# Optimization experiments

Measured on AMD Instinct MI355X. Metric: run time of the kernel, lower is better.

## Reference

```python
import jax, jax.numpy as jnp
import numpy as np

B, T, C = 2, 2048, 2048
NH, NKV, HD = 16, 8, 256
SOFTCAP = 50.0
ROPE_BASE = 10000.0


def setup_inputs() -> dict:
    key = jax.random.key(0)
    ks = jax.random.split(key, 5)
    s = 0.02
    return {
        "X": jax.random.normal(ks[0], (B, T, C), dtype=jnp.float32),
        "Wq": jax.random.normal(ks[1], (C, NH * HD), dtype=jnp.float32) * s,
        "Wk": jax.random.normal(ks[2], (C, NKV * HD), dtype=jnp.float32) * s,
        "Wv": jax.random.normal(ks[3], (C, NKV * HD), dtype=jnp.float32) * s,
        "Wo": jax.random.normal(ks[4], (NH * HD, C), dtype=jnp.float32) * s,
    }


def _rotate_half(x):
    x1, x2 = x[..., : x.shape[-1] // 2], x[..., x.shape[-1] // 2 :]
    return jnp.concatenate((-x2, x1), axis=-1)


def _rope_cos_sin(t, head_dim, dtype):
    inv_freq = 1.0 / ROPE_BASE ** (
        jnp.arange(0, head_dim, 2, dtype=jnp.int32).astype(jnp.float32) / head_dim
    )  # [HD/2]
    pos = jnp.arange(t, dtype=jnp.float32)  # [T]
    freqs = pos[:, None] * inv_freq[None, :]  # [T, HD/2]
    emb = jnp.concatenate((freqs, freqs), axis=-1)  # [T, HD]
    # shape [1, 1, T, HD] to broadcast over (B, H, T, HD)
    return (
        jnp.cos(emb).astype(dtype)[None, None],
        jnp.sin(emb).astype(dtype)[None, None],
    )


def reference(X, Wq, Wk, Wv, Wo):
    b, t, c = X.shape
    n_rep = NH // NKV

    q = (X @ Wq).reshape(b, t, NH, HD).transpose(0, 2, 1, 3)   # [B,NH,T,HD]
    k = (X @ Wk).reshape(b, t, NKV, HD).transpose(0, 2, 1, 3)  # [B,NKV,T,HD]
    v = (X @ Wv).reshape(b, t, NKV, HD).transpose(0, 2, 1, 3)

    cos, sin = _rope_cos_sin(t, HD, X.dtype)
    q = q * cos + _rotate_half(q) * sin
    k = k * cos + _rotate_half(k) * sin

    # repeat_kv (GQA): [B,NKV,T,HD] -> [B,NH,T,HD]
    k = jnp.repeat(k, n_rep, axis=1)
    v = jnp.repeat(v, n_rep, axis=1)

    scale = 256.0 ** (-0.5)  # hardcoded in source
    att = jnp.einsum("bhqd,bhkd->bhqk", q, k) * scale
    # tanh logit softcapping
    att = SOFTCAP * jnp.tanh(att / SOFTCAP)
    # causal mask
    causal = jnp.tril(jnp.ones((t, t), dtype=bool))
    att = jnp.where(causal[None, None], att, -jnp.inf)
    att = jax.nn.softmax(att, axis=-1)

    y = jnp.einsum("bhqk,bhkd->bhqd", att, v)  # [B,NH,T,HD]
    y = y.transpose(0, 2, 1, 3).reshape(b, t, NH * HD)
    return y @ Wo
```

## Files before the change

### kernel.cpp

```cpp
#include <hip/hip_runtime.h>
#include <hip/hip_bf16.h>

#define NHD 16
#define NKVH 8
#define HDIM 256
#define TSEQ 2048
#define BATCH 2

typedef unsigned int   u32;
typedef unsigned short u16;

typedef __attribute__((ext_vector_type(8))) short bf16x8;
typedef __attribute__((ext_vector_type(4))) float floatx4;

__device__ inline u32 cvt2bf(float lo, float hi) {
  u32 r;
  asm("v_cvt_pk_bf16_f32 %0, %1, %2" : "=v"(r) : "v"(lo), "v"(hi));
  return r;
}
__device__ inline u16 f2bf(float f) {
  union { float f; u32 i; } v; v.f = f;
  u32 r = v.i + 0x7fffu + ((v.i >> 16) & 1u);
  return (u16)(r >> 16);
}
__device__ inline float bf2f(u16 u) {
  union { u32 i; float f; } v; v.i = ((u32)u) << 16; return v.f;
}
__device__ inline float fexp2(float x) {
  float r; asm("v_exp_f32 %0, %1" : "=v"(r) : "v"(x)); return r;
}
__device__ inline float frcp(float x) {
  float r; asm("v_rcp_f32 %0, %1" : "=v"(r) : "v"(x)); return r;
}

typedef const __attribute__((address_space(1))) u32* gptr_t;
typedef __attribute__((address_space(3))) u32* lptr_t;
__device__ inline void gl_lds16(const void* g, void* l) {
  __builtin_amdgcn_global_load_lds((gptr_t)g, (lptr_t)l, 16, 0, 0);
}

__global__ __launch_bounds__(256) void tconv_k(
    const float* __restrict__ in, u16* __restrict__ out, int R, int Cc)
{
  __shared__ float tile[64][65];
  const int r0 = blockIdx.y * 64, c0 = blockIdx.x * 64;
  const int tr = threadIdx.x >> 4;
  const int tc = (threadIdx.x & 15) * 4;
#pragma unroll
  for (int j = 0; j < 4; ++j) {
    float4 v = *(const float4*)(in + (size_t)(r0 + tr + j * 16) * Cc + c0 + tc);
    tile[tr + j * 16][tc + 0] = v.x;
    tile[tr + j * 16][tc + 1] = v.y;
    tile[tr + j * 16][tc + 2] = v.z;
    tile[tr + j * 16][tc + 3] = v.w;
  }
  __syncthreads();
#pragma unroll
  for (int j = 0; j < 4; ++j) {
    int c = tr + j * 16;
    u16 o[4];
#pragma unroll
    for (int i = 0; i < 4; ++i) o[i] = f2bf(tile[tc + i][c]);
    *(uint2*)(out + (size_t)(c0 + c) * R + r0 + tc) = *(const uint2*)o;
  }
}

__global__ __launch_bounds__(256) void xconv_k(
    const float* __restrict__ in, u16* __restrict__ out)
{
  size_t i = (size_t)blockIdx.x * 256 + threadIdx.x;
  float4 a = *(const float4*)(in + i * 8);
  float4 b = *(const float4*)(in + i * 8 + 4);
  uint4 o;
  o.x = cvt2bf(a.x, a.y); o.y = cvt2bf(a.z, a.w);
  o.z = cvt2bf(b.x, b.y); o.w = cvt2bf(b.z, b.w);
  *(uint4*)(out + i * 8) = o;
}

template<int EPI, int BM>
__global__ __launch_bounds__(512, 2) void gemm256_k(
    const u16* __restrict__ Ab, const u16* __restrict__ BTp,
    void* __restrict__ Op, int M, int N, int K)
{
  constexpr int NI = BM / 32;
  constexpr int AI = BM / 64;
  __shared__ u16 LA[2][BM * 64];
  __shared__ u16 LB[2][256 * 64];
  const int t = threadIdx.x;
  const int lane = t & 63, wave = t >> 6;
  const int lg = lane >> 4, l15 = lane & 15;
  const int wm = wave >> 2, wn = wave & 3;
  const int mtiles = M / BM;
  const int mt = (int)blockIdx.x % mtiles, nt = (int)blockIdx.x / mtiles;
  const int m0 = mt * BM, n0 = nt << 8;

  const int arow = wave * (BM / 8) + (lane >> 3);
  const int ska  = ((lane & 7) ^ (arow & 7)) << 3;
  const int brow = wave * 32 + (lane >> 3);
  const int skb  = ((lane & 7) ^ (brow & 7)) << 3;
  const u16* Ag = Ab  + (size_t)(m0 + arow) * K + ska;
  const u16* Bg = BTp + (size_t)(n0 + brow) * K + skb;

  auto STAGE = [&](int k0, int sel) {
#pragma unroll
    for (int q = 0; q < AI; ++q)
      gl_lds16(Ag + k0 + (size_t)q * 8 * K, &LA[sel][(wave * (BM / 8) + q * 8) * 64]);
#pragma unroll
    for (int q = 0; q < 4; ++q)
      gl_lds16(Bg + k0 + (size_t)q * 8 * K, &LB[sel][(wave * 32 + q * 8) * 64]);
  };

  floatx4 acc[NI][4];
#pragma unroll
  for (int i = 0; i < NI; ++i)
#pragma unroll
    for (int j = 0; j < 4; ++j) acc[i][j] = (floatx4){0.f, 0.f, 0.f, 0.f};

  STAGE(0, 0);
  const int KT = K >> 6;
  for (int kt = 0; kt < KT; ++kt) {
    const int sel = kt & 1;
    if (kt + 1 < KT) {
      STAGE((kt + 1) << 6, sel ^ 1);
      if constexpr (BM == 256) asm volatile("s_waitcnt vmcnt(8)" ::: "memory");
      else                     asm volatile("s_waitcnt vmcnt(6)" ::: "memory");
    } else {
      asm volatile("s_waitcnt vmcnt(0)" ::: "memory");
    }
    __builtin_amdgcn_s_barrier();
    __builtin_amdgcn_sched_barrier(0);
    __builtin_amdgcn_s_setprio(1);
#pragma unroll
    for (int ks = 0; ks < 2; ++ks) {
      const int c = (ks << 2) + lg;
      bf16x8 bfv[4];
#pragma unroll
      for (int j = 0; j < 4; ++j) {
        int row = wn * 64 + (j << 4) + l15;
        bfv[j] = *(const bf16x8*)(&LB[sel][row * 64 + ((c ^ (row & 7)) << 3)]);
      }
#pragma unroll
      for (int i = 0; i < NI; ++i) {
        int row = wm * (BM / 2) + (i << 4) + l15;
        bf16x8 af = *(const bf16x8*)(&LA[sel][row * 64 + ((c ^ (row & 7)) << 3)]);
#pragma unroll
        for (int j = 0; j < 4; ++j)
          acc[i][j] = __builtin_amdgcn_mfma_f32_16x16x32_bf16(af, bfv[j], acc[i][j], 0, 0, 0);
      }
    }
    __builtin_amdgcn_s_setprio(0);
    __builtin_amdgcn_s_barrier();
  }

#pragma unroll
  for (int i = 0; i < NI; ++i) {
#pragma unroll
    for (int j = 0; j < 4; ++j) {
#pragma unroll
      for (int r = 0; r < 4; ++r) {
        int m = m0 + wm * (BM / 2) + (i << 4) + (lg << 2) + r;
        int n = n0 + wn * 64 + (j << 4) + l15;
        float v = acc[i][j][r];
        int bb = m >> 11, tt = m & 2047;
        if (EPI == 0) {
          ((float*)Op)[(size_t)m * N + n] = v;
        } else if (EPI == 1) {
          int h = n >> 8, d = n & 255;
          ((u16*)Op)[(((size_t)bb * NHD + h) * TSEQ + tt) * HDIM + d] = f2bf(v);
        } else {
          if (n < 2048) {
            int h = n >> 8, d = n & 255;
            ((u16*)Op)[(((size_t)bb * NKVH + h) * TSEQ + tt) * HDIM + d] = f2bf(v);
          } else {
            int n2 = n - 2048;
            int h = n2 >> 8, d = n2 & 255;
            ((u16*)Op)[8388608u + (((size_t)bb * NKVH + h) * HDIM + d) * TSEQ + tt] = f2bf(v);
          }
        }
      }
    }
  }
}

__global__ __launch_bounds__(256) void rope_k(u16* buf) {
  size_t idx = (size_t)blockIdx.x * 256 + threadIdx.x;
  int d = (int)(idx & 127);
  size_t rest = idx >> 7;
  int tt = (int)(rest & (TSEQ - 1));
  float invf = exp2f(-(float)d * 0.103810253f);
  float th = (float)tt * invf;
  float sn, cs;
  sincosf(th, &sn, &cs);
  size_t base = rest * HDIM;
  float x1 = bf2f(buf[base + d]);
  float x2 = bf2f(buf[base + d + 128]);
  buf[base + d]       = f2bf(x1 * cs - x2 * sn);
  buf[base + d + 128] = f2bf(x2 * cs + x1 * sn);
}

__global__ __launch_bounds__(256, 2) void attn_k(
    const u16* __restrict__ Q, const u16* __restrict__ Kb,
    const u16* __restrict__ Vt, u16* __restrict__ Y)
{
  __shared__ u16 Ks2[2][32 * 256];
  __shared__ u16 Vs2[2][256 * 32];
  __shared__ u16 Ps[4 * 16 * 32];
  __shared__ float Ls[4][16];
  const int t = threadIdx.x, lane = t & 63, w = t >> 6;
  const int lg = lane >> 4, l15 = lane & 15;
  const int qt = 31 - (int)blockIdx.y;
  const int h = (int)blockIdx.x >> 1, b = (int)blockIdx.x & 1;
  const int hkv = h >> 1;

  const u16* Kg = Kb + ((size_t)(b * NKVH + hkv)) * TSEQ * HDIM;
  const u16* Vg = Vt + ((size_t)(b * NKVH + hkv)) * HDIM * TSEQ;

  int koff[4], voff[4];
#pragma unroll
  for (int q = 0; q < 4; ++q) {
    int krow = w * 8 + q * 2 + (lane >> 5);
    int kcc  = lane & 31;
    koff[q] = krow * 256 + ((kcc ^ (krow & 7)) << 3);
    int vd  = w * 64 + q * 16 + (lane >> 2);
    voff[q] = vd * TSEQ + (((lane & 3) ^ ((vd >> 2) & 3)) << 3);
  }

  auto STAGE = [&](int st, int sel) {
    const u16* kbase = Kg + (size_t)st * (32 * 256);
    const u16* vbase = Vg + st * 32;
#pragma unroll
    for (int q = 0; q < 4; ++q)
      gl_lds16(kbase + koff[q], &Ks2[sel][(w * 8 + q * 2) * 256]);
#pragma unroll
    for (int q = 0; q < 4; ++q)
      gl_lds16(vbase + voff[q], &Vs2[sel][(w * 64 + q * 16) * 32]);
  };

  const u16* Qg = Q + (((size_t)(b * NHD + h)) * TSEQ + qt * 64 + w * 16 + l15) * HDIM;
  bf16x8 qf[8];
#pragma unroll
  for (int ks = 0; ks < 8; ++ks) qf[ks] = *(const bf16x8*)(Qg + ks * 32 + lg * 8);

  floatx4 accY[16];
#pragma unroll
  for (int i = 0; i < 16; ++i) accY[i] = (floatx4){0.f, 0.f, 0.f, 0.f};
  float rsum = 0.f;

  const int qglob = qt * 64 + w * 16 + l15;
  const int qmaxw = qt * 64 + w * 16 + 15;
  const int nst = 2 * qt + 2;
  const int fps = (l15 ^ (l15 >> 2)) & 3;

  STAGE(0, 0);
  for (int st = 0; st < nst; ++st) {
    const int sel = st & 1;
    if (st + 1 < nst) {
      STAGE(st + 1, sel ^ 1);
      asm volatile("s_waitcnt vmcnt(8)" ::: "memory");
    } else {
      asm volatile("s_waitcnt vmcnt(0)" ::: "memory");
    }
    __builtin_amdgcn_s_barrier();
    __builtin_amdgcn_sched_barrier(0);

    if (st * 32 <= qmaxw) {
      __builtin_amdgcn_s_setprio(1);
#pragma unroll
      for (int stile = 0; stile < 2; ++stile) {
        floatx4 sa = (floatx4){0.f, 0.f, 0.f, 0.f};
#pragma unroll
        for (int ks = 0; ks < 8; ++ks) {
          int row = (stile << 4) + l15;
          int c = (ks << 2) + lg;
          bf16x8 kf = *(const bf16x8*)((const char*)Ks2[sel] +
                        row * 512 + ((c ^ (row & 7)) << 4));
          sa = __builtin_amdgcn_mfma_f32_16x16x32_bf16(kf, qf[ks], sa, 0, 0, 0);
        }
        int sbase = st * 32 + (stile << 4) + (lg << 2);
        float p[4];
#pragma unroll
        for (int r = 0; r < 4; ++r) {
          float u = fexp2(sa[r] * 0.0036067376f);
          float pv = fexp2(-144.26950408f * frcp(u + 1.0f));
          pv = (sbase + r <= qglob) ? pv : 0.0f;
          p[r] = pv;
          rsum += pv;
        }
        uint2 pw;
        pw.x = cvt2bf(p[0], p[1]);
        pw.y = cvt2bf(p[2], p[3]);
        int o = (stile << 5) + (lg << 3);
        int gran = (o >> 4) ^ fps;
        *(uint2*)((char*)Ps + (w << 10) + l15 * 64 + (gran << 4) + (o & 15)) = pw;
      }
      {
        bf16x8 pf = *(const bf16x8*)((const char*)Ps + (w << 10) + l15 * 64 +
                      ((lg ^ fps) << 4));
#pragma unroll
        for (int dt = 0; dt < 16; ++dt) {
          int row = (dt << 4) + l15;
          bf16x8 vf = *(const bf16x8*)((const char*)Vs2[sel] +
                        row * 64 + ((lg ^ ((row >> 2) & 3)) << 4));
          accY[dt] = __builtin_amdgcn_mfma_f32_16x16x32_bf16(pf, vf, accY[dt], 0, 0, 0);
        }
      }
      __builtin_amdgcn_s_setprio(0);
    }
    __builtin_amdgcn_s_barrier();
  }

  rsum += __shfl_xor(rsum, 16);
  rsum += __shfl_xor(rsum, 32);
  if (lane < 16) Ls[w][l15] = rsum;
  __syncthreads();
  float inv[4];
#pragma unroll
  for (int r = 0; r < 4; ++r) inv[r] = 1.0f / Ls[w][(lg << 2) + r];

  u16* Yg = Y + ((size_t)(b * TSEQ + qt * 64 + w * 16)) * (NHD * HDIM) + h * HDIM;
#pragma unroll
  for (int dt = 0; dt < 16; ++dt)
#pragma unroll
    for (int r = 0; r < 4; ++r)
      Yg[(size_t)((lg << 2) + r) * (NHD * HDIM) + (dt << 4) + l15] =
          f2bf(accY[dt][r] * inv[r]);
}

extern "C" void kernel_launch(void* const* d_in, const int* in_sizes, int n_in,
                              void* d_out, int out_size, void* d_ws, size_t ws_size,
                              hipStream_t stream) {
  const float* X  = (const float*)d_in[0];
  const float* Wq = (const float*)d_in[1];
  const float* Wk = (const float*)d_in[2];
  const float* Wv = (const float*)d_in[3];
  const float* Wo = (const float*)d_in[4];
  float* out = (float*)d_out;

  u16* ws   = (u16*)d_ws;
  u16* XB   = ws;
  u16* WT   = ws + 8388608;
  u16* Qb   = ws + 16777216;
  u16* KVb  = ws + 33554432;
  u16* Yb   = ws;
  u16* WoT  = ws + 16777216;

  dim3 blk(256);
  xconv_k<<<dim3(4096), blk, 0, stream>>>(X, XB);
  tconv_k<<<dim3(64, 32), blk, 0, stream>>>(Wq, WT, 2048, 4096);
  gemm256_k<1, 256><<<dim3(16 * 16), dim3(512), 0, stream>>>(XB, WT, Qb, 4096, 4096, 2048);
  tconv_k<<<dim3(32, 32), blk, 0, stream>>>(Wk, WT, 2048, 2048);
  tconv_k<<<dim3(32, 32), blk, 0, stream>>>(Wv, WT + (size_t)2048 * 2048, 2048, 2048);
  gemm256_k<3, 256><<<dim3(16 * 16), dim3(512), 0, stream>>>(XB, WT, KVb, 4096, 4096, 2048);
  rope_k<<<dim3((BATCH * NHD  * TSEQ * 128) / 256), blk, 0, stream>>>(Qb);
  rope_k<<<dim3((BATCH * NKVH * TSEQ * 128) / 256), blk, 0, stream>>>(KVb);
  attn_k<<<dim3(32, 32), blk, 0, stream>>>(Qb, KVb, KVb + 8388608, Yb);
  tconv_k<<<dim3(32, 64), blk, 0, stream>>>(Wo, WoT, 4096, 2048);
  gemm256_k<0, 128><<<dim3(32 * 8), dim3(512), 0, stream>>>(Yb, WoT, out, 4096, 2048, 4096);
}
```

Baseline: 424.9 us.

## Share K/V tiles across both GQA query heads and split GEMM B-tile staging

The attention kernel now processes both query heads that share a KV head in one block. Each staged K/V tile is reused twice and the grid is halved, which cuts global K/V traffic and staging work. This doubles the Q fragment and Y accumulator registers per thread, so occupancy may drop or registers may spill. Separately, the GEMM prefetch now issues the next A tile before compute and the next B tile between the two k-substeps. The vmcnt waits are adjusted to match, so load issue interleaves with MFMA work.

Result: slower. 680.7 us (+60.2%).

```diff
diff --git a/kernel.cpp b/kernel.cpp
--- a/kernel.cpp
+++ b/kernel.cpp
@@ -101,10 +101,12 @@
   const u16* Ag = Ab  + (size_t)(m0 + arow) * K + ska;
   const u16* Bg = BTp + (size_t)(n0 + brow) * K + skb;
 
-  auto STAGE = [&](int k0, int sel) {
+  auto STAGE_A = [&](int k0, int sel) {
 #pragma unroll
     for (int q = 0; q < AI; ++q)
       gl_lds16(Ag + k0 + (size_t)q * 8 * K, &LA[sel][(wave * (BM / 8) + q * 8) * 64]);
+  };
+  auto STAGE_B = [&](int k0, int sel) {
 #pragma unroll
     for (int q = 0; q < 4; ++q)
       gl_lds16(Bg + k0 + (size_t)q * 8 * K, &LB[sel][(wave * 32 + q * 8) * 64]);
@@ -116,23 +118,46 @@
 #pragma unroll
     for (int j = 0; j < 4; ++j) acc[i][j] = (floatx4){0.f, 0.f, 0.f, 0.f};
 
-  STAGE(0, 0);
+  STAGE_A(0, 0);
+  STAGE_B(0, 0);
   const int KT = K >> 6;
   for (int kt = 0; kt < KT; ++kt) {
     const int sel = kt & 1;
     if (kt + 1 < KT) {
-      STAGE((kt + 1) << 6, sel ^ 1);
-      if constexpr (BM == 256) asm volatile("s_waitcnt vmcnt(8)" ::: "memory");
-      else                     asm volatile("s_waitcnt vmcnt(6)" ::: "memory");
+      STAGE_A((kt + 1) << 6, sel ^ 1);
+      if constexpr (BM == 256) asm volatile("s_waitcnt vmcnt(4)" ::: "memory");
+      else                     asm volatile("s_waitcnt vmcnt(2)" ::: "memory");
     } else {
       asm volatile("s_waitcnt vmcnt(0)" ::: "memory");
     }
     __builtin_amdgcn_s_barrier();
     __builtin_amdgcn_sched_barrier(0);
+
     __builtin_amdgcn_s_setprio(1);
-#pragma unroll
-    for (int ks = 0; ks < 2; ++ks) {
-      const int c = (ks << 2) + lg;
+    {
+      const int c = lg;
+      bf16x8 bfv[4];
+#pragma unroll
+      for (int j = 0; j < 4; ++j) {
+        int row = wn * 64 + (j << 4) + l15;
+        bfv[j] = *(const bf16x8*)(&LB[sel][row * 64 + ((c ^ (row & 7)) << 3)]);
+      }
+#pragma unroll
+      for (int i = 0; i < NI; ++i) {
+        int row = wm * (BM / 2) + (i << 4) + l15;
+        bf16x8 af = *(const bf16x8*)(&LA[sel][row * 64 + ((c ^ (row & 7)) << 3)]);
+#pragma unroll
+        for (int j = 0; j < 4; ++j)
+          acc[i][j] = __builtin_amdgcn_mfma_f32_16x16x32_bf16(af, bfv[j], acc[i][j], 0, 0, 0);
+      }
+    }
+    __builtin_amdgcn_s_setprio(0);
+
+    if (kt + 1 < KT) STAGE_B((kt + 1) << 6, sel ^ 1);
+
+    __builtin_amdgcn_s_setprio(1);
+    {
+      const int c = 4 + lg;
       bf16x8 bfv[4];
 #pragma unroll
       for (int j = 0; j < 4; ++j) {
@@ -205,12 +230,11 @@
   __shared__ u16 Ks2[2][32 * 256];
   __shared__ u16 Vs2[2][256 * 32];
   __shared__ u16 Ps[4 * 16 * 32];
-  __shared__ float Ls[4][16];
+  __shared__ float Ls[4][2][16];
   const int t = threadIdx.x, lane = t & 63, w = t >> 6;
   const int lg = lane >> 4, l15 = lane & 15;
   const int qt = 31 - (int)blockIdx.y;
-  const int h = (int)blockIdx.x >> 1, b = (int)blockIdx.x & 1;
-  const int hkv = h >> 1;
+  const int hkv = (int)blockIdx.x >> 1, b = (int)blockIdx.x & 1;
 
   const u16* Kg = Kb + ((size_t)(b * NKVH + hkv)) * TSEQ * HDIM;
   const u16* Vg = Vt + ((size_t)(b * NKVH + hkv)) * HDIM * TSEQ;
@@ -236,15 +260,22 @@
       gl_lds16(vbase + voff[q], &Vs2[sel][(w * 64 + q * 16) * 32]);
   };
 
-  const u16* Qg = Q + (((size_t)(b * NHD + h)) * TSEQ + qt * 64 + w * 16 + l15) * HDIM;
-  bf16x8 qf[8];
-#pragma unroll
-  for (int ks = 0; ks < 8; ++ks) qf[ks] = *(const bf16x8*)(Qg + ks * 32 + lg * 8);
-
-  floatx4 accY[16];
-#pragma unroll
-  for (int i = 0; i < 16; ++i) accY[i] = (floatx4){0.f, 0.f, 0.f, 0.f};
-  float rsum = 0.f;
+  bf16x8 qf[2][8];
+#pragma unroll
+  for (int u = 0; u < 2; ++u) {
+    const u16* Qg = Q + (((size_t)(b * NHD + 2 * hkv + u)) * TSEQ +
+                         qt * 64 + w * 16 + l15) * HDIM;
+#pragma unroll
+    for (int ks = 0; ks < 8; ++ks)
+      qf[u][ks] = *(const bf16x8*)(Qg + ks * 32 + lg * 8);
+  }
+
+  floatx4 accY[2][16];
+#pragma unroll
+  for (int u = 0; u < 2; ++u)
+#pragma unroll
+    for (int i = 0; i < 16; ++i) accY[u][i] = (floatx4){0.f, 0.f, 0.f, 0.f};
+  float rsum[2] = {0.f, 0.f};
 
   const int qglob = qt * 64 + w * 16 + l15;
   const int qmaxw = qt * 64 + w * 16 + 15;
@@ -266,64 +297,74 @@
     if (st * 32 <= qmaxw) {
       __builtin_amdgcn_s_setprio(1);
 #pragma unroll
-      for (int stile = 0; stile < 2; ++stile) {
-        floatx4 sa = (floatx4){0.f, 0.f, 0.f, 0.f};
-#pragma unroll
-        for (int ks = 0; ks < 8; ++ks) {
-          int row = (stile << 4) + l15;
-          int c = (ks << 2) + lg;
-          bf16x8 kf = *(const bf16x8*)((const char*)Ks2[sel] +
-                        row * 512 + ((c ^ (row & 7)) << 4));
-          sa = __builtin_amdgcn_mfma_f32_16x16x32_bf16(kf, qf[ks], sa, 0, 0, 0);
+      for (int u = 0; u < 2; ++u) {
+#pragma unroll
+        for (int stile = 0; stile < 2; ++stile) {
+          floatx4 sa = (floatx4){0.f, 0.f, 0.f, 0.f};
+#pragma unroll
+          for (int ks = 0; ks < 8; ++ks) {
+            int row = (stile << 4) + l15;
+            int c = (ks << 2) + lg;
+            bf16x8 kf = *(const bf16x8*)((const char*)Ks2[sel] +
+                          row * 512 + ((c ^ (row & 7)) << 4));
+            sa = __builtin_amdgcn_mfma_f32_16x16x32_bf16(kf, qf[u][ks], sa, 0, 0, 0);
+          }
+          int sbase = st * 32 + (stile << 4) + (lg << 2);
+          float p[4];
+#pragma unroll
+          for (int r = 0; r < 4; ++r) {
+            float uu = fexp2(sa[r] * 0.0036067376f);
+            float pv = fexp2(-144.26950408f * frcp(uu + 1.0f));
+            pv = (sbase + r <= qglob) ? pv : 0.0f;
+            p[r] = pv;
+            rsum[u] += pv;
+          }
+          uint2 pw;
+          pw.x = cvt2bf(p[0], p[1]);
+          pw.y = cvt2bf(p[2], p[3]);
+          int o = (stile << 5) + (lg << 3);
+          int gran = (o >> 4) ^ fps;
+          *(uint2*)((char*)Ps + (w << 10) + l15 * 64 + (gran << 4) + (o & 15)) = pw;
         }
-        int sbase = st * 32 + (stile << 4) + (lg << 2);
-        float p[4];
-#pragma unroll
-        for (int r = 0; r < 4; ++r) {
-          float u = fexp2(sa[r] * 0.0036067376f);
-          float pv = fexp2(-144.26950408f * frcp(u + 1.0f));
-          pv = (sbase + r <= qglob) ? pv : 0.0f;
-          p[r] = pv;
-          rsum += pv;
+        {
+          bf16x8 pf = *(const bf16x8*)((const char*)Ps + (w << 10) + l15 * 64 +
+                        ((lg ^ fps) << 4));
+#pragma unroll
+          for (int dt = 0; dt < 16; ++dt) {
+            int row = (dt << 4) + l15;
+            bf16x8 vf = *(const bf16x8*)((const char*)Vs2[sel] +
+                          row * 64 + ((lg ^ ((row >> 2) & 3)) << 4));
+            accY[u][dt] = __builtin_amdgcn_mfma_f32_16x16x32_bf16(pf, vf, accY[u][dt], 0, 0, 0);
+          }
         }
-        uint2 pw;
-        pw.x = cvt2bf(p[0], p[1]);
-        pw.y = cvt2bf(p[2], p[3]);
-        int o = (stile << 5) + (lg << 3);
-        int gran = (o >> 4) ^ fps;
-        *(uint2*)((char*)Ps + (w << 10) + l15 * 64 + (gran << 4) + (o & 15)) = pw;
-      }
-      {
-        bf16x8 pf = *(const bf16x8*)((const char*)Ps + (w << 10) + l15 * 64 +
-                      ((lg ^ fps) << 4));
-#pragma unroll
-        for (int dt = 0; dt < 16; ++dt) {
-          int row = (dt << 4) + l15;
-          bf16x8 vf = *(const bf16x8*)((const char*)Vs2[sel] +
-                        row * 64 + ((lg ^ ((row >> 2) & 3)) << 4));
-          accY[dt] = __builtin_amdgcn_mfma_f32_16x16x32_bf16(pf, vf, accY[dt], 0, 0, 0);
-        }
       }
       __builtin_amdgcn_s_setprio(0);
     }
     __builtin_amdgcn_s_barrier();
   }
 
-  rsum += __shfl_xor(rsum, 16);
-  rsum += __shfl_xor(rsum, 32);
-  if (lane < 16) Ls[w][l15] = rsum;
+#pragma unroll
+  for (int u = 0; u < 2; ++u) {
+    float rs = rsum[u];
+    rs += __shfl_xor(rs, 16);
+    rs += __shfl_xor(rs, 32);
+    if (lane < 16) Ls[w][u][l15] = rs;
+  }
   __syncthreads();
-  float inv[4];
-#pragma unroll
-  for (int r = 0; r < 4; ++r) inv[r] = 1.0f / Ls[w][(lg << 2) + r];
-
-  u16* Yg = Y + ((size_t)(b * TSEQ + qt * 64 + w * 16)) * (NHD * HDIM) + h * HDIM;
-#pragma unroll
-  for (int dt = 0; dt < 16; ++dt)
-#pragma unroll
-    for (int r = 0; r < 4; ++r)
-      Yg[(size_t)((lg << 2) + r) * (NHD * HDIM) + (dt << 4) + l15] =
-          f2bf(accY[dt][r] * inv[r]);
+#pragma unroll
+  for (int u = 0; u < 2; ++u) {
+    float inv[4];
+#pragma unroll
+    for (int r = 0; r < 4; ++r) inv[r] = 1.0f / Ls[w][u][(lg << 2) + r];
+    u16* Yg = Y + ((size_t)(b * TSEQ + qt * 64 + w * 16)) * (NHD * HDIM) +
+              (2 * hkv + u) * HDIM;
+#pragma unroll
+    for (int dt = 0; dt < 16; ++dt)
+#pragma unroll
+      for (int r = 0; r < 4; ++r)
+        Yg[(size_t)((lg << 2) + r) * (NHD * HDIM) + (dt << 4) + l15] =
+            f2bf(accY[u][dt][r] * inv[r]);
+  }
 }
 
 extern "C" void kernel_launch(void* const* d_in, const int* in_sizes, int n_in,
@@ -353,7 +394,7 @@
   gemm256_k<3, 256><<<dim3(16 * 16), dim3(512), 0, stream>>>(XB, WT, KVb, 4096, 4096, 2048);
   rope_k<<<dim3((BATCH * NHD  * TSEQ * 128) / 256), blk, 0, stream>>>(Qb);
   rope_k<<<dim3((BATCH * NKVH * TSEQ * 128) / 256), blk, 0, stream>>>(KVb);
-  attn_k<<<dim3(32, 32), blk, 0, stream>>>(Qb, KVb, KVb + 8388608, Yb);
+  attn_k<<<dim3(16, 32), blk, 0, stream>>>(Qb, KVb, KVb + 8388608, Yb);
   tconv_k<<<dim3(32, 64), blk, 0, stream>>>(Wo, WoT, 4096, 2048);
   gemm256_k<0, 128><<<dim3(32 * 8), dim3(512), 0, stream>>>(Yb, WoT, out, 4096, 2048, 4096);
 }
```

## Restructure GEMM into four-phase pipelined loop with k-group-major LDS layout

Applied to the files above, without the earlier changes.

The GEMM kernel now stores its LDS tiles k-group-major (8-element column groups laid out contiguously across rows) instead of an XOR-swizzled row-major layout. The global-to-LDS prefetch of the next k-tile is split across four phases inside each k-iteration, interleaved with LDS fragment loads and half-tile MFMA batches separated by barriers. The goal is to spread memory traffic across the compute, hide load latency and avoid LDS bank conflicts. In exchange it adds more barriers per iteration and changes the global access pattern, with each lane loading a different row.

Result: slower. 512.0 us (+20.5%).

```diff
diff --git a/kernel.cpp b/kernel.cpp
--- a/kernel.cpp
+++ b/kernel.cpp
@@ -78,14 +78,18 @@
 }
 
 template<int EPI, int BM>
-__global__ __launch_bounds__(512, 2) void gemm256_k(
+__global__ __launch_bounds__(512, 2) void gemmp_k(
     const u16* __restrict__ Ab, const u16* __restrict__ BTp,
     void* __restrict__ Op, int M, int N, int K)
 {
-  constexpr int NI = BM / 32;
-  constexpr int AI = BM / 64;
-  __shared__ u16 LA[2][BM * 64];
-  __shared__ u16 LB[2][256 * 64];
+  constexpr int NI   = BM / 32;
+  constexpr int NH2  = NI / 2;
+  constexpr int ATOT = BM / 64;
+  constexpr int ST   = ATOT + 4;
+  constexpr int ASZ  = BM * 64;
+  constexpr int BSZ  = 256 * 64;
+  __shared__ u16 LA[2 * ASZ];
+  __shared__ u16 LB[2 * BSZ];
   const int t = threadIdx.x;
   const int lane = t & 63, wave = t >> 6;
   const int lg = lane >> 4, l15 = lane & 15;
@@ -94,20 +98,18 @@
   const int mt = (int)blockIdx.x % mtiles, nt = (int)blockIdx.x / mtiles;
   const int m0 = mt * BM, n0 = nt << 8;
 
-  const int arow = wave * (BM / 8) + (lane >> 3);
-  const int ska  = ((lane & 7) ^ (arow & 7)) << 3;
-  const int brow = wave * 32 + (lane >> 3);
-  const int skb  = ((lane & 7) ^ (brow & 7)) << 3;
-  const u16* Ag = Ab  + (size_t)(m0 + arow) * K + ska;
-  const u16* Bg = BTp + (size_t)(n0 + brow) * K + skb;
-
-  auto STAGE = [&](int k0, int sel) {
-#pragma unroll
-    for (int q = 0; q < AI; ++q)
-      gl_lds16(Ag + k0 + (size_t)q * 8 * K, &LA[sel][(wave * (BM / 8) + q * 8) * 64]);
-#pragma unroll
-    for (int q = 0; q < 4; ++q)
-      gl_lds16(Bg + k0 + (size_t)q * 8 * K, &LB[sel][(wave * 32 + q * 8) * 64]);
+  auto STAGE1 = [&](int idx, int k0, int sel) {
+    if (idx < ATOT) {
+      int gi = wave * ATOT + idx;
+      int g = gi & 7, rc = gi >> 3;
+      gl_lds16(Ab + (size_t)(m0 + rc * 64 + lane) * K + k0 + g * 8,
+               &LA[sel * ASZ + (g * BM + rc * 64) * 8]);
+    } else {
+      int gi = wave * 4 + (idx - ATOT);
+      int g = gi & 7, rc = gi >> 3;
+      gl_lds16(BTp + (size_t)(n0 + rc * 64 + lane) * K + k0 + g * 8,
+               &LB[sel * BSZ + (g * 256 + rc * 64) * 8]);
+    }
   };
 
   floatx4 acc[NI][4];
@@ -116,40 +118,51 @@
 #pragma unroll
     for (int j = 0; j < 4; ++j) acc[i][j] = (floatx4){0.f, 0.f, 0.f, 0.f};
 
-  STAGE(0, 0);
+#pragma unroll
+  for (int idx = 0; idx < ST; ++idx) STAGE1(idx, 0, 0);
+  asm volatile("s_waitcnt vmcnt(0)" ::: "memory");
+  __builtin_amdgcn_s_barrier();
+
   const int KT = K >> 6;
   for (int kt = 0; kt < KT; ++kt) {
     const int sel = kt & 1;
-    if (kt + 1 < KT) {
-      STAGE((kt + 1) << 6, sel ^ 1);
-      if constexpr (BM == 256) asm volatile("s_waitcnt vmcnt(8)" ::: "memory");
-      else                     asm volatile("s_waitcnt vmcnt(6)" ::: "memory");
-    } else {
-      asm volatile("s_waitcnt vmcnt(0)" ::: "memory");
-    }
-    __builtin_amdgcn_s_barrier();
-    __builtin_amdgcn_sched_barrier(0);
-    __builtin_amdgcn_s_setprio(1);
-#pragma unroll
-    for (int ks = 0; ks < 2; ++ks) {
-      const int c = (ks << 2) + lg;
-      bf16x8 bfv[4];
-#pragma unroll
-      for (int j = 0; j < 4; ++j) {
-        int row = wn * 64 + (j << 4) + l15;
-        bfv[j] = *(const bf16x8*)(&LB[sel][row * 64 + ((c ^ (row & 7)) << 3)]);
-      }
-#pragma unroll
-      for (int i = 0; i < NI; ++i) {
-        int row = wm * (BM / 2) + (i << 4) + l15;
-        bf16x8 af = *(const bf16x8*)(&LA[sel][row * 64 + ((c ^ (row & 7)) << 3)]);
+    const int k1 = (kt + 1) << 6;
+    bf16x8 bfv[4];
+#pragma unroll
+    for (int p = 0; p < 4; ++p) {
+      const int ih = p & 1, ks = p >> 1;
+      if (ih == 0) {
+#pragma unroll
+        for (int j = 0; j < 4; ++j) {
+          int row = wn * 64 + (j << 4) + l15;
+          bfv[j] = *(const bf16x8*)(&LB[sel * BSZ + (((ks << 2) + lg) * 256 + row) * 8]);
+        }
+      }
+      bf16x8 af[NH2];
+#pragma unroll
+      for (int i = 0; i < NH2; ++i) {
+        int row = wm * (BM / 2) + ((ih * NH2 + i) << 4) + l15;
+        af[i] = *(const bf16x8*)(&LA[sel * ASZ + (((ks << 2) + lg) * BM + row) * 8]);
+      }
+      if (kt + 1 < KT) {
+#pragma unroll
+        for (int idx = (p * ST) >> 2; idx < ((p + 1) * ST) >> 2; ++idx)
+          STAGE1(idx, k1, sel ^ 1);
+      }
+      __builtin_amdgcn_s_barrier();
+      asm volatile("s_waitcnt lgkmcnt(0)" ::: "memory");
+      __builtin_amdgcn_sched_barrier(0);
+      __builtin_amdgcn_s_setprio(1);
+#pragma unroll
+      for (int i = 0; i < NH2; ++i)
 #pragma unroll
         for (int j = 0; j < 4; ++j)
-          acc[i][j] = __builtin_amdgcn_mfma_f32_16x16x32_bf16(af, bfv[j], acc[i][j], 0, 0, 0);
-      }
-    }
-    __builtin_amdgcn_s_setprio(0);
-    __builtin_amdgcn_s_barrier();
+          acc[ih * NH2 + i][j] =
+              __builtin_amdgcn_mfma_f32_16x16x32_bf16(af[i], bfv[j], acc[ih * NH2 + i][j], 0, 0, 0);
+      __builtin_amdgcn_s_setprio(0);
+      if (p == 3) asm volatile("s_waitcnt vmcnt(0)" ::: "memory");
+      __builtin_amdgcn_s_barrier();
+    }
   }
 
 #pragma unroll
@@ -347,13 +360,13 @@
   dim3 blk(256);
   xconv_k<<<dim3(4096), blk, 0, stream>>>(X, XB);
   tconv_k<<<dim3(64, 32), blk, 0, stream>>>(Wq, WT, 2048, 4096);
-  gemm256_k<1, 256><<<dim3(16 * 16), dim3(512), 0, stream>>>(XB, WT, Qb, 4096, 4096, 2048);
+  gemmp_k<1, 256><<<dim3(16 * 16), dim3(512), 0, stream>>>(XB, WT, Qb, 4096, 4096, 2048);
   tconv_k<<<dim3(32, 32), blk, 0, stream>>>(Wk, WT, 2048, 2048);
   tconv_k<<<dim3(32, 32), blk, 0, stream>>>(Wv, WT + (size_t)2048 * 2048, 2048, 2048);
-  gemm256_k<3, 256><<<dim3(16 * 16), dim3(512), 0, stream>>>(XB, WT, KVb, 4096, 4096, 2048);
+  gemmp_k<3, 256><<<dim3(16 * 16), dim3(512), 0, stream>>>(XB, WT, KVb, 4096, 4096, 2048);
   rope_k<<<dim3((BATCH * NHD  * TSEQ * 128) / 256), blk, 0, stream>>>(Qb);
   rope_k<<<dim3((BATCH * NKVH * TSEQ * 128) / 256), blk, 0, stream>>>(KVb);
   attn_k<<<dim3(32, 32), blk, 0, stream>>>(Qb, KVb, KVb + 8388608, Yb);
   tconv_k<<<dim3(32, 64), blk, 0, stream>>>(Wo, WoT, 4096, 2048);
-  gemm256_k<0, 128><<<dim3(32 * 8), dim3(512), 0, stream>>>(Yb, WoT, out, 4096, 2048, 4096);
-}
+  gemmp_k<0, 128><<<dim3(32 * 8), dim3(512), 0, stream>>>(Yb, WoT, out, 4096, 2048, 4096);
+}
```

## Restructure GEMM into 4-slot K=32 pipeline with grouped LDS layout and block swizzle

Applied to the files above, without the earlier changes.

Replaces the double-buffered K=64 GEMM loop with a 4-slot ring of K=32 stages that keeps three loads in flight. The LDS layout changes from an XOR-swizzled row layout to one grouped by k-chunk, and fragments are loaded before the next stage is issued. It also remaps block IDs across 8 groups, likely to spread tiles across XCDs or improve cache locality. The aim is deeper prefetch to hide global latency, at the cost of twice as many barriers per K, and the new LDS layout may bring bank conflicts.

Measured after the change: 462.1 us. 8.8% more time.

```diff
diff --git a/kernel.cpp b/kernel.cpp
--- a/kernel.cpp
+++ b/kernel.cpp
@@ -78,36 +78,46 @@
 }
 
 template<int EPI, int BM>
-__global__ __launch_bounds__(512, 2) void gemm256_k(
+__global__ __launch_bounds__(512, 2) void gemmp2_k(
     const u16* __restrict__ Ab, const u16* __restrict__ BTp,
     void* __restrict__ Op, int M, int N, int K)
 {
-  constexpr int NI = BM / 32;
-  constexpr int AI = BM / 64;
-  __shared__ u16 LA[2][BM * 64];
-  __shared__ u16 LB[2][256 * 64];
+  constexpr int NI  = BM / 32;
+  constexpr int AIN = BM / 128;
+  constexpr int ASL = BM * 32;
+  constexpr int BSL = 256 * 32;
+  __shared__ u16 LA[4 * ASL];
+  __shared__ u16 LB[4 * BSL];
   const int t = threadIdx.x;
   const int lane = t & 63, wave = t >> 6;
   const int lg = lane >> 4, l15 = lane & 15;
   const int wm = wave >> 2, wn = wave & 3;
   const int mtiles = M / BM;
-  const int mt = (int)blockIdx.x % mtiles, nt = (int)blockIdx.x / mtiles;
+  const int nwg = (int)gridDim.x;
+  int bid = (int)blockIdx.x;
+  bid = (bid & 7) * (nwg >> 3) + (bid >> 3);
+  const int mt = bid % mtiles, nt = bid / mtiles;
   const int m0 = mt * BM, n0 = nt << 8;
 
-  const int arow = wave * (BM / 8) + (lane >> 3);
-  const int ska  = ((lane & 7) ^ (arow & 7)) << 3;
-  const int brow = wave * 32 + (lane >> 3);
-  const int skb  = ((lane & 7) ^ (brow & 7)) << 3;
-  const u16* Ag = Ab  + (size_t)(m0 + arow) * K + ska;
-  const u16* Bg = BTp + (size_t)(n0 + brow) * K + skb;
-
-  auto STAGE = [&](int k0, int sel) {
-#pragma unroll
-    for (int q = 0; q < AI; ++q)
-      gl_lds16(Ag + k0 + (size_t)q * 8 * K, &LA[sel][(wave * (BM / 8) + q * 8) * 64]);
-#pragma unroll
-    for (int q = 0; q < 4; ++q)
-      gl_lds16(Bg + k0 + (size_t)q * 8 * K, &LB[sel][(wave * 32 + q * 8) * 64]);
+  const int NHALF = K >> 5;
+
+  auto STAGE = [&](int H) {
+    const int slot = H & 3;
+    const int k0 = H << 5;
+#pragma unroll
+    for (int q = 0; q < AIN; ++q) {
+      int idx = wave * AIN + q;
+      int g = idx & 3, rc = idx >> 2;
+      gl_lds16(Ab + (size_t)(m0 + rc * 64 + lane) * K + k0 + g * 8,
+               &LA[slot * ASL + (g * BM + rc * 64) * 8]);
+    }
+#pragma unroll
+    for (int q = 0; q < 2; ++q) {
+      int idx = wave * 2 + q;
+      int g = idx & 3, rc = idx >> 2;
+      gl_lds16(BTp + (size_t)(n0 + rc * 64 + lane) * K + k0 + g * 8,
+               &LB[slot * BSL + (g * 256 + rc * 64) * 8]);
+    }
   };
 
   floatx4 acc[NI][4];
@@ -116,38 +126,40 @@
 #pragma unroll
     for (int j = 0; j < 4; ++j) acc[i][j] = (floatx4){0.f, 0.f, 0.f, 0.f};
 
-  STAGE(0, 0);
-  const int KT = K >> 6;
-  for (int kt = 0; kt < KT; ++kt) {
-    const int sel = kt & 1;
-    if (kt + 1 < KT) {
-      STAGE((kt + 1) << 6, sel ^ 1);
-      if constexpr (BM == 256) asm volatile("s_waitcnt vmcnt(8)" ::: "memory");
-      else                     asm volatile("s_waitcnt vmcnt(6)" ::: "memory");
+  STAGE(0); STAGE(1); STAGE(2);
+
+  for (int H = 0; H < NHALF; ++H) {
+    const int slot = H & 3;
+    const int rem = NHALF - 1 - H;
+    if constexpr (BM == 256) {
+      if (rem >= 2)      asm volatile("s_waitcnt vmcnt(8)" ::: "memory");
+      else if (rem == 1) asm volatile("s_waitcnt vmcnt(4)" ::: "memory");
+      else               asm volatile("s_waitcnt vmcnt(0)" ::: "memory");
     } else {
-      asm volatile("s_waitcnt vmcnt(0)" ::: "memory");
+      if (rem >= 2)      asm volatile("s_waitcnt vmcnt(6)" ::: "memory");
+      else if (rem == 1) asm volatile("s_waitcnt vmcnt(3)" ::: "memory");
+      else               asm volatile("s_waitcnt vmcnt(0)" ::: "memory");
     }
     __builtin_amdgcn_s_barrier();
+
+    bf16x8 bfv[4], af[NI];
+#pragma unroll
+    for (int j = 0; j < 4; ++j)
+      bfv[j] = *(const bf16x8*)(&LB[slot * BSL + (lg * 256 + wn * 64 + (j << 4) + l15) * 8]);
+#pragma unroll
+    for (int i = 0; i < NI; ++i)
+      af[i] = *(const bf16x8*)(&LA[slot * ASL + (lg * BM + wm * (BM / 2) + (i << 4) + l15) * 8]);
+
+    if (H + 3 < NHALF) STAGE(H + 3);
+
+    asm volatile("s_waitcnt lgkmcnt(0)" ::: "memory");
     __builtin_amdgcn_sched_barrier(0);
     __builtin_amdgcn_s_setprio(1);
 #pragma unroll
-    for (int ks = 0; ks < 2; ++ks) {
-      const int c = (ks << 2) + lg;
-      bf16x8 bfv[4];
-#pragma unroll
-      for (int j = 0; j < 4; ++j) {
-        int row = wn * 64 + (j << 4) + l15;
-        bfv[j] = *(const bf16x8*)(&LB[sel][row * 64 + ((c ^ (row & 7)) << 3)]);
-      }
-#pragma unroll
-      for (int i = 0; i < NI; ++i) {
-        int row = wm * (BM / 2) + (i << 4) + l15;
-        bf16x8 af = *(const bf16x8*)(&LA[sel][row * 64 + ((c ^ (row & 7)) << 3)]);
-#pragma unroll
-        for (int j = 0; j < 4; ++j)
-          acc[i][j] = __builtin_amdgcn_mfma_f32_16x16x32_bf16(af, bfv[j], acc[i][j], 0, 0, 0);
-      }
-    }
+    for (int i = 0; i < NI; ++i)
+#pragma unroll
+      for (int j = 0; j < 4; ++j)
+        acc[i][j] = __builtin_amdgcn_mfma_f32_16x16x32_bf16(af[i], bfv[j], acc[i][j], 0, 0, 0);
     __builtin_amdgcn_s_setprio(0);
     __builtin_amdgcn_s_barrier();
   }
@@ -347,13 +359,13 @@
   dim3 blk(256);
   xconv_k<<<dim3(4096), blk, 0, stream>>>(X, XB);
   tconv_k<<<dim3(64, 32), blk, 0, stream>>>(Wq, WT, 2048, 4096);
-  gemm256_k<1, 256><<<dim3(16 * 16), dim3(512), 0, stream>>>(XB, WT, Qb, 4096, 4096, 2048);
+  gemmp2_k<1, 256><<<dim3(16 * 16), dim3(512), 0, stream>>>(XB, WT, Qb, 4096, 4096, 2048);
   tconv_k<<<dim3(32, 32), blk, 0, stream>>>(Wk, WT, 2048, 2048);
   tconv_k<<<dim3(32, 32), blk, 0, stream>>>(Wv, WT + (size_t)2048 * 2048, 2048, 2048);
-  gemm256_k<3, 256><<<dim3(16 * 16), dim3(512), 0, stream>>>(XB, WT, KVb, 4096, 4096, 2048);
+  gemmp2_k<3, 256><<<dim3(16 * 16), dim3(512), 0, stream>>>(XB, WT, KVb, 4096, 4096, 2048);
   rope_k<<<dim3((BATCH * NHD  * TSEQ * 128) / 256), blk, 0, stream>>>(Qb);
   rope_k<<<dim3((BATCH * NKVH * TSEQ * 128) / 256), blk, 0, stream>>>(KVb);
   attn_k<<<dim3(32, 32), blk, 0, stream>>>(Qb, KVb, KVb + 8388608, Yb);
   tconv_k<<<dim3(32, 64), blk, 0, stream>>>(Wo, WoT, 4096, 2048);
-  gemm256_k<0, 128><<<dim3(32 * 8), dim3(512), 0, stream>>>(Yb, WoT, out, 4096, 2048, 4096);
-}
+  gemmp2_k<0, 128><<<dim3(32 * 8), dim3(512), 0, stream>>>(Yb, WoT, out, 4096, 2048, 4096);
+}
```
